# Performance work log

Measured on AMD Instinct MI355X. Metric: run time of the kernel, lower is better.

Reference implementation:

```python
import jax, jax.numpy as jnp
import numpy as np

N_NODES = 100000
N_EDGES = 1600000
D_IN = 128
D_OUT = 128


def setup_inputs() -> dict:
    key = jax.random.key(0)
    ks = jax.random.split(key, 8)
    h = jax.random.normal(ks[0], (N_NODES, D_IN), dtype=jnp.float32)
    edge_val = jax.random.uniform(ks[1], (N_EDGES,), dtype=jnp.float32)
    # Linear weights in torch layout [out, in]
    W_self = jax.random.normal(ks[2], (D_OUT, D_IN), dtype=jnp.float32) * (1.0 / np.sqrt(D_IN))
    b_self = jax.random.normal(ks[3], (D_OUT,), dtype=jnp.float32) * 0.01
    W_nb = jax.random.normal(ks[4], (D_OUT, D_IN), dtype=jnp.float32) * (1.0 / np.sqrt(D_IN))
    b_nb = jax.random.normal(ks[5], (D_OUT,), dtype=jnp.float32) * 0.01
    edge_row = jax.random.randint(ks[6], (N_EDGES,), 0, N_NODES, dtype=jnp.int64)
    edge_col = jax.random.randint(ks[7], (N_EDGES,), 0, N_NODES, dtype=jnp.int64)
    return {"h": h, "edge_val": edge_val, "W_self": W_self, "b_self": b_self,
            "W_nb": W_nb, "b_nb": b_nb, "edge_row": edge_row, "edge_col": edge_col}


def reference(h, edge_val, W_self, b_self, W_nb, b_nb, edge_row, edge_col):
    # self_h = Linear_self(h[:out_nodes]); out_nodes == N_NODES here
    self_h = h @ W_self.T + b_self  # [N, D_OUT]
    # neighbor_h = adj.spmm(h): sparse COO (row, col, val) times dense h
    msgs = edge_val[:, None] * h[edge_col]            # [E, D_IN]
    neighbor_h = jax.ops.segment_sum(msgs, edge_row, num_segments=N_NODES)  # [N, D_IN]
    out = self_h + neighbor_h @ W_nb.T + b_nb
    return out
```

## Files before the change

### kernel.cpp

```cpp
#include <hip/hip_runtime.h>


constexpr int NN = 100000;
constexpr int NE = 1600000;
constexpr int D  = 128;
constexpr int NBUCK  = 500;
constexpr int BROWS  = 200;
constexpr int BCAP   = 3584;
constexpr int CHUNK  = 2048;
constexpr int NCH    = (NE + CHUNK - 1) / CHUNK;
constexpr int GM     = 64;
constexpr int NT     = (NN + GM - 1) / GM;
constexpr int GRID   = 512;
constexpr int LP     = 132;

typedef __bf16 bf16x8 __attribute__((ext_vector_type(8)));
typedef float  f32x4  __attribute__((ext_vector_type(4)));
typedef float  f32x2  __attribute__((ext_vector_type(2)));
typedef unsigned short u16x4 __attribute__((ext_vector_type(4)));

__global__ __launch_bounds__(256) void gemm_mfma(
    const float* __restrict__ h,
    const float* __restrict__ Wself,
    const float* __restrict__ Wnb,
    const float* __restrict__ bself,
    const float* __restrict__ bnb,
    float* __restrict__ out,
    __bf16* __restrict__ tmpb)
{
    __shared__ __bf16 hs[2][GM * LP];
    const int t    = threadIdx.x;
    const int w    = t >> 6;
    const int lane = t & 63;
    const int l15  = lane & 15;
    const int quad = lane >> 4;

    bf16x8 wf[4][4];
    #pragma unroll
    for (int ns = 0; ns < 4; ++ns) {
        int wrow = w * 64 + ns * 16 + l15;
        const float* wr = (wrow < D) ? (Wself + (size_t)wrow * D)
                                     : (Wnb + (size_t)(wrow - D) * D);
        #pragma unroll
        for (int kk = 0; kk < 4; ++kk) {
            f32x4 lo = *(const f32x4*)(wr + kk * 32 + quad * 8);
            f32x4 hi = *(const f32x4*)(wr + kk * 32 + quad * 8 + 4);
            bf16x8 bb;
            #pragma unroll
            for (int j = 0; j < 4; ++j) { bb[j] = (__bf16)lo[j]; bb[4 + j] = (__bf16)hi[j]; }
            wf[ns][kk] = bb;
        }
    }
    f32x4 biasv[4];
    #pragma unroll
    for (int ns = 0; ns < 4; ++ns) {
        int col = w * 64 + ns * 16 + quad * 4;
        if (col < D) {
            f32x4 b1 = *(const f32x4*)(bself + col);
            f32x4 b2 = *(const f32x4*)(bnb + col);
            biasv[ns] = b1 + b2;
        } else biasv[ns] = (f32x4){0.f, 0.f, 0.f, 0.f};
    }

    int srow[4], scol[4];
    #pragma unroll
    for (int it = 0; it < 4; ++it) {
        int idx = it * 2048 + t * 8;
        srow[it] = idx >> 7;
        scol[it] = idx & 127;
    }

    {
        const int row0 = blockIdx.x * GM;
        #pragma unroll
        for (int it = 0; it < 4; ++it) {
            int gr = row0 + srow[it]; if (gr >= NN) gr = NN - 1;
            f32x4 lo = *(const f32x4*)(h + (size_t)gr * D + scol[it]);
            f32x4 hi = *(const f32x4*)(h + (size_t)gr * D + scol[it] + 4);
            bf16x8 v;
            #pragma unroll
            for (int j = 0; j < 4; ++j) { v[j] = (__bf16)lo[j]; v[4 + j] = (__bf16)hi[j]; }
            *(bf16x8*)(&hs[0][srow[it] * LP + scol[it]]) = v;
        }
    }
    __syncthreads();

    int buf = 0;
    for (int tile = blockIdx.x; tile < NT; tile += GRID) {
        const int row0 = tile * GM;
        const bool hasn = (tile + GRID) < NT;

        f32x4 pf[8];
        if (hasn) {
            const int nrow0 = (tile + GRID) * GM;
            #pragma unroll
            for (int it = 0; it < 4; ++it) {
                int gr = nrow0 + srow[it]; if (gr >= NN) gr = NN - 1;
                pf[it * 2]     = *(const f32x4*)(h + (size_t)gr * D + scol[it]);
                pf[it * 2 + 1] = *(const f32x4*)(h + (size_t)gr * D + scol[it] + 4);
            }
        }

        f32x4 acc[4][4];
        #pragma unroll
        for (int mi = 0; mi < 4; ++mi)
            #pragma unroll
            for (int ns = 0; ns < 4; ++ns) acc[mi][ns] = (f32x4){0.f, 0.f, 0.f, 0.f};

        const __bf16* hb = hs[buf];
        #pragma unroll
        for (int mi = 0; mi < 4; ++mi) {
            bf16x8 hf[4];
            #pragma unroll
            for (int kk = 0; kk < 4; ++kk)
                hf[kk] = *(const bf16x8*)(&hb[(mi * 16 + l15) * LP + quad * 8 + kk * 32]);
            #pragma unroll
            for (int ns = 0; ns < 4; ++ns)
                #pragma unroll
                for (int kk = 0; kk < 4; ++kk)
                    acc[mi][ns] = __builtin_amdgcn_mfma_f32_16x16x32_bf16(wf[ns][kk], hf[kk], acc[mi][ns], 0, 0, 0);
        }

        if (hasn) {
            #pragma unroll
            for (int it = 0; it < 4; ++it) {
                bf16x8 v;
                #pragma unroll
                for (int j = 0; j < 4; ++j) {
                    v[j]     = (__bf16)pf[it * 2][j];
                    v[4 + j] = (__bf16)pf[it * 2 + 1][j];
                }
                *(bf16x8*)(&hs[buf ^ 1][srow[it] * LP + scol[it]]) = v;
            }
        }
        __syncthreads();

        #pragma unroll
        for (int mi = 0; mi < 4; ++mi) {
            int row = row0 + mi * 16 + l15;
            if (row < NN) {
                if (w < 2) {
                    #pragma unroll
                    for (int ns = 0; ns < 4; ++ns) {
                        int col = w * 64 + ns * 16 + quad * 4;
                        *(f32x4*)(out + (size_t)row * D + col) = acc[mi][ns] + biasv[ns];
                    }
                } else {
                    #pragma unroll
                    for (int ns = 0; ns < 4; ++ns) {
                        int col = (w - 2) * 64 + ns * 16 + quad * 4;
                        u16x4 v;
                        #pragma unroll
                        for (int i = 0; i < 4; ++i) {
                            __bf16 b = (__bf16)acc[mi][ns][i];
                            v[i] = *(unsigned short*)&b;
                        }
                        *(u16x4*)(tmpb + (size_t)row * D + col) = v;
                    }
                }
            }
        }
        buf ^= 1;
    }
}

__global__ __launch_bounds__(256) void wc_scatter(
    const int* __restrict__ erow, const int* __restrict__ ecol,
    const float* __restrict__ eval_,
    int* __restrict__ gcount, int2* __restrict__ epair)
{
    __shared__ int  cnt[NBUCK];
    __shared__ int  lscan[NBUCK];
    __shared__ int  gbase[NBUCK];
    __shared__ int  ss[512];
    __shared__ int2 sbuf[CHUNK];
    __shared__ int  saddr[CHUNK];
    __shared__ int  s_total;

    const int t  = threadIdx.x;
    const int c0 = blockIdx.x * CHUNK;

    for (int b = t; b < NBUCK; b += 256) cnt[b] = 0;
    __syncthreads();

    int   bp[8];
    int   colr[8];
    float valr[8];
    #pragma unroll
    for (int j = 0; j < 8; ++j) {
        int e = c0 + j * 256 + t;
        if (e < NE) {
            int r   = erow[e];
            colr[j] = ecol[e];
            valr[j] = eval_[e];
            int b   = r / BROWS;
            int rlo = r - b * BROWS;
            int pos = atomicAdd(&cnt[b], 1);
            bp[j]   = b | (rlo << 9) | (pos << 17);
        } else bp[j] = -1;
    }
    __syncthreads();

    ss[t]       = (t < NBUCK)       ? cnt[t]       : 0;
    ss[t + 256] = (t + 256 < NBUCK) ? cnt[t + 256] : 0;
    __syncthreads();
    for (int off = 1; off < 512; off <<= 1) {
        int i0 = t, i1 = t + 256;
        int r0 = ss[i0] + ((i0 >= off) ? ss[i0 - off] : 0);
        int r1 = ss[i1] + ((i1 >= off) ? ss[i1 - off] : 0);
        __syncthreads();
        ss[i0] = r0; ss[i1] = r1;
        __syncthreads();
    }
    if (t < NBUCK) {
        int n = cnt[t];
        lscan[t] = ss[t] - n;
        gbase[t] = (n > 0) ? atomicAdd(&gcount[t], n) : 0;
    }
    if (t + 256 < NBUCK) {
        int n = cnt[t + 256];
        lscan[t + 256] = ss[t + 256] - n;
        gbase[t + 256] = (n > 0) ? atomicAdd(&gcount[t + 256], n) : 0;
    }
    if (t == 0) s_total = ss[511];
    __syncthreads();

    #pragma unroll
    for (int j = 0; j < 8; ++j) {
        if (bp[j] >= 0) {
            int b   = bp[j] & 511;
            int rlo = (bp[j] >> 9) & 255;
            int pos = bp[j] >> 17;
            int slot = lscan[b] + pos;
            sbuf[slot]  = make_int2(colr[j] | (rlo << 17), __float_as_int(valr[j]));
            saddr[slot] = b * BCAP + gbase[b] + pos;
        }
    }
    __syncthreads();

    int ce = s_total;
    for (int i = t; i < ce; i += 256)
        epair[saddr[i]] = sbuf[i];
}

__global__ __launch_bounds__(512) void bucket_sort(
    const int2* __restrict__ epair, const int* __restrict__ gcount,
    int2* __restrict__ epair2, int2* __restrict__ rowrange)
{
    __shared__ int  cnt[BROWS];
    __shared__ int  off2[BROWS];
    __shared__ int  cur[BROWS];
    __shared__ int  ss[256];
    __shared__ int2 sorted[BCAP];

    const int t = threadIdx.x;
    const int b = blockIdx.x;
    const int n = gcount[b];
    const int2* src = epair + (size_t)b * BCAP;

    if (t < BROWS) cnt[t] = 0;
    __syncthreads();

    int2 r[8];
    int  nr = 0;
    for (int i = t; i < n; i += 512) {
        int2 p = src[i];
        r[nr++] = p;
        atomicAdd(&cnt[(p.x >> 17) & 255], 1);
    }
    __syncthreads();

    if (t < 256) ss[t] = (t < BROWS) ? cnt[t] : 0;
    __syncthreads();
    for (int o = 1; o < 256; o <<= 1) {
        int y = 0;
        if (t < 256 && t >= o) y = ss[t - o];
        __syncthreads();
        if (t < 256) ss[t] += y;
        __syncthreads();
    }
    if (t < BROWS) {
        int v = cnt[t];
        off2[t] = ss[t] - v;
        cur[t]  = ss[t] - v;
    }
    __syncthreads();

    for (int j = 0; j < nr; ++j) {
        int slot = atomicAdd(&cur[(r[j].x >> 17) & 255], 1);
        sorted[slot] = r[j];
    }
    __syncthreads();

    const int base = b * BCAP;
    for (int i = t; i < n; i += 512)
        epair2[base + i] = sorted[i];
    if (t < BROWS) {
        int row = b * BROWS + t;
        if (row < NN)
            rowrange[row] = make_int2(base + off2[t], base + off2[t] + cnt[t]);
    }
}

__global__ __launch_bounds__(256) void aggregate(
    const __bf16* __restrict__ tmpb, const int2* __restrict__ rowrange,
    const int2* __restrict__ epair2, float* __restrict__ out,
    int row0, int nrows)
{
    int wave = row0 + ((blockIdx.x * 256 + threadIdx.x) >> 6);
    if (wave >= row0 + nrows) return;
    int lane = threadIdx.x & 63;
    int2 rr = rowrange[wave];
    int beg = __builtin_amdgcn_readfirstlane(rr.x);
    int end = __builtin_amdgcn_readfirstlane(rr.y);

    float ax[4] = {0.f, 0.f, 0.f, 0.f};
    float ay[4] = {0.f, 0.f, 0.f, 0.f};
    int e = beg;
    for (; e + 7 < end; e += 8) {
        int2 p[8];
        #pragma unroll
        for (int k = 0; k < 8; ++k) p[k] = epair2[e + k];
        #pragma unroll
        for (int k = 0; k < 8; ++k) {
            int col = p[k].x & 0x1FFFF;
            unsigned u = *(const unsigned*)(tmpb + (size_t)col * D + lane * 2);
            float v = __int_as_float(p[k].y);
            ax[k & 3] += v * __uint_as_float(u << 16);
            ay[k & 3] += v * __uint_as_float(u & 0xffff0000u);
        }
    }
    for (; e + 3 < end; e += 4) {
        int2 p[4];
        #pragma unroll
        for (int k = 0; k < 4; ++k) p[k] = epair2[e + k];
        #pragma unroll
        for (int k = 0; k < 4; ++k) {
            int col = p[k].x & 0x1FFFF;
            unsigned u = *(const unsigned*)(tmpb + (size_t)col * D + lane * 2);
            float v = __int_as_float(p[k].y);
            ax[k] += v * __uint_as_float(u << 16);
            ay[k] += v * __uint_as_float(u & 0xffff0000u);
        }
    }
    for (; e < end; ++e) {
        int2 p = epair2[e];
        int col = p.x & 0x1FFFF;
        unsigned u = *(const unsigned*)(tmpb + (size_t)col * D + lane * 2);
        float v = __int_as_float(p.y);
        ax[0] += v * __uint_as_float(u << 16);
        ay[0] += v * __uint_as_float(u & 0xffff0000u);
    }
    f32x2* o = (f32x2*)(out + (size_t)wave * D + lane * 2);
    f32x2 c = __builtin_nontemporal_load(o);
    c.x += (ax[0] + ax[1]) + (ax[2] + ax[3]);
    c.y += (ay[0] + ay[1]) + (ay[2] + ay[3]);
    __builtin_nontemporal_store(c, o);
}

extern "C" void kernel_launch(void* const* d_in, const int* in_sizes, int n_in,
                              void* d_out, int out_size, void* d_ws, size_t ws_size,
                              hipStream_t stream) {
    const float* h     = (const float*)d_in[0];
    const float* eval_ = (const float*)d_in[1];
    const float* Wself = (const float*)d_in[2];
    const float* bself = (const float*)d_in[3];
    const float* Wnb   = (const float*)d_in[4];
    const float* bnb   = (const float*)d_in[5];
    const int*   erow  = (const int*)d_in[6];
    const int*   ecol  = (const int*)d_in[7];
    float* out = (float*)d_out;

    char* p = (char*)d_ws;
    __bf16* tmpb    = (__bf16*)p;   p += (size_t)NT * GM * D * 2;
    int2*   epair   = (int2*)p;     p += (size_t)NBUCK * BCAP * 8;
    int2*   epair2  = (int2*)p;     p += (size_t)NBUCK * BCAP * 8;
    int2*   rowrange= (int2*)p;     p += (size_t)NN * 8;
    int*    gcount  = (int*)p;

    hipMemsetAsync(gcount, 0, NBUCK * 4, stream);

    gemm_mfma<<<GRID, 256, 0, stream>>>(h, Wself, Wnb, bself, bnb, out, tmpb);
    wc_scatter<<<NCH, 256, 0, stream>>>(erow, ecol, eval_, gcount, epair);
    bucket_sort<<<NBUCK, 512, 0, stream>>>(epair, gcount, epair2, rowrange);
    aggregate<<<(NN * 64) / 256, 256, 0, stream>>>(tmpb, rowrange, epair2, out, 0, NN);
}
```

Baseline: 251.8 us.

## Fuse bucket sort with neighbor aggregation, reading sorted edges from LDS

Merges the per-bucket counting sort and the SpMM aggregation into one kernel. Each block sorts its bucket's edges in shared memory, then its 8 waves each aggregate 25 rows straight from the LDS-resident sorted list. This removes the global round-trip of epair2 and rowrange and one kernel launch. In exchange, aggregation parallelism drops to 500 blocks of 8 waves each processing 25 rows sequentially, which may reduce latency hiding and cause load imbalance compared with one wave per row. The large LDS footprint also limits how many blocks can be resident per CU.

```diff
diff --git a/kernel.cpp b/kernel.cpp
--- a/kernel.cpp
+++ b/kernel.cpp
@@ -243,9 +243,9 @@
         epair[saddr[i]] = sbuf[i];
 }
 
-__global__ __launch_bounds__(512) void bucket_sort(
+__global__ __launch_bounds__(512, 4) void sort_aggregate(
     const int2* __restrict__ epair, const int* __restrict__ gcount,
-    int2* __restrict__ epair2, int2* __restrict__ rowrange)
+    const __bf16* __restrict__ tmpb, float* __restrict__ out)
 {
     __shared__ int  cnt[BROWS];
     __shared__ int  off2[BROWS];
@@ -292,70 +292,60 @@
     }
     __syncthreads();
 
-    const int base = b * BCAP;
-    for (int i = t; i < n; i += 512)
-        epair2[base + i] = sorted[i];
-    if (t < BROWS) {
-        int row = b * BROWS + t;
-        if (row < NN)
-            rowrange[row] = make_int2(base + off2[t], base + off2[t] + cnt[t]);
-    }
-}
-
-__global__ __launch_bounds__(256) void aggregate(
-    const __bf16* __restrict__ tmpb, const int2* __restrict__ rowrange,
-    const int2* __restrict__ epair2, float* __restrict__ out,
-    int row0, int nrows)
-{
-    int wave = row0 + ((blockIdx.x * 256 + threadIdx.x) >> 6);
-    if (wave >= row0 + nrows) return;
-    int lane = threadIdx.x & 63;
-    int2 rr = rowrange[wave];
-    int beg = __builtin_amdgcn_readfirstlane(rr.x);
-    int end = __builtin_amdgcn_readfirstlane(rr.y);
-
-    float ax[4] = {0.f, 0.f, 0.f, 0.f};
-    float ay[4] = {0.f, 0.f, 0.f, 0.f};
-    int e = beg;
-    for (; e + 7 < end; e += 8) {
-        int2 p[8];
-        #pragma unroll
-        for (int k = 0; k < 8; ++k) p[k] = epair2[e + k];
-        #pragma unroll
-        for (int k = 0; k < 8; ++k) {
-            int col = p[k].x & 0x1FFFF;
-            unsigned u = *(const unsigned*)(tmpb + (size_t)col * D + lane * 2);
-            float v = __int_as_float(p[k].y);
-            ax[k & 3] += v * __uint_as_float(u << 16);
-            ay[k & 3] += v * __uint_as_float(u & 0xffff0000u);
-        }
-    }
-    for (; e + 3 < end; e += 4) {
-        int2 p[4];
-        #pragma unroll
-        for (int k = 0; k < 4; ++k) p[k] = epair2[e + k];
-        #pragma unroll
-        for (int k = 0; k < 4; ++k) {
-            int col = p[k].x & 0x1FFFF;
-            unsigned u = *(const unsigned*)(tmpb + (size_t)col * D + lane * 2);
-            float v = __int_as_float(p[k].y);
-            ax[k] += v * __uint_as_float(u << 16);
-            ay[k] += v * __uint_as_float(u & 0xffff0000u);
-        }
-    }
-    for (; e < end; ++e) {
-        int2 p = epair2[e];
-        int col = p.x & 0x1FFFF;
-        unsigned u = *(const unsigned*)(tmpb + (size_t)col * D + lane * 2);
-        float v = __int_as_float(p.y);
-        ax[0] += v * __uint_as_float(u << 16);
-        ay[0] += v * __uint_as_float(u & 0xffff0000u);
-    }
-    f32x2* o = (f32x2*)(out + (size_t)wave * D + lane * 2);
-    f32x2 c = __builtin_nontemporal_load(o);
-    c.x += (ax[0] + ax[1]) + (ax[2] + ax[3]);
-    c.y += (ay[0] + ay[1]) + (ay[2] + ay[3]);
-    __builtin_nontemporal_store(c, o);
+    const int wv   = t >> 6;
+    const int lane = t & 63;
+    const __bf16* tb = tmpb + lane * 2;
+
+    for (int rl = wv * 25; rl < wv * 25 + 25; ++rl) {
+        int beg = __builtin_amdgcn_readfirstlane(off2[rl]);
+        int end = __builtin_amdgcn_readfirstlane(cur[rl]);
+        if (beg >= end) continue;
+
+        float ax[4] = {0.f, 0.f, 0.f, 0.f};
+        float ay[4] = {0.f, 0.f, 0.f, 0.f};
+        int e = beg;
+        for (; e + 7 < end; e += 8) {
+            int2 p[8];
+            #pragma unroll
+            for (int k = 0; k < 8; ++k) p[k] = sorted[e + k];
+            #pragma unroll
+            for (int k = 0; k < 8; ++k) {
+                int col = p[k].x & 0x1FFFF;
+                unsigned u = *(const unsigned*)(tb + (size_t)col * D);
+                float v = __int_as_float(p[k].y);
+                ax[k & 3] += v * __uint_as_float(u << 16);
+                ay[k & 3] += v * __uint_as_float(u & 0xffff0000u);
+            }
+        }
+        for (; e + 3 < end; e += 4) {
+            int2 p[4];
+            #pragma unroll
+            for (int k = 0; k < 4; ++k) p[k] = sorted[e + k];
+            #pragma unroll
+            for (int k = 0; k < 4; ++k) {
+                int col = p[k].x & 0x1FFFF;
+                unsigned u = *(const unsigned*)(tb + (size_t)col * D);
+                float v = __int_as_float(p[k].y);
+                ax[k] += v * __uint_as_float(u << 16);
+                ay[k] += v * __uint_as_float(u & 0xffff0000u);
+            }
+        }
+        for (; e < end; ++e) {
+            int2 p = sorted[e];
+            int col = p.x & 0x1FFFF;
+            unsigned u = *(const unsigned*)(tb + (size_t)col * D);
+            float v = __int_as_float(p.y);
+            ax[0] += v * __uint_as_float(u << 16);
+            ay[0] += v * __uint_as_float(u & 0xffff0000u);
+        }
+
+        int row = b * BROWS + rl;
+        f32x2* o = (f32x2*)(out + (size_t)row * D + lane * 2);
+        f32x2 c = __builtin_nontemporal_load(o);
+        c.x += (ax[0] + ax[1]) + (ax[2] + ax[3]);
+        c.y += (ay[0] + ay[1]) + (ay[2] + ay[3]);
+        __builtin_nontemporal_store(c, o);
+    }
 }
 
 extern "C" void kernel_launch(void* const* d_in, const int* in_sizes, int n_in,
@@ -374,14 +364,11 @@
     char* p = (char*)d_ws;
     __bf16* tmpb    = (__bf16*)p;   p += (size_t)NT * GM * D * 2;
     int2*   epair   = (int2*)p;     p += (size_t)NBUCK * BCAP * 8;
-    int2*   epair2  = (int2*)p;     p += (size_t)NBUCK * BCAP * 8;
-    int2*   rowrange= (int2*)p;     p += (size_t)NN * 8;
     int*    gcount  = (int*)p;
 
     hipMemsetAsync(gcount, 0, NBUCK * 4, stream);
 
     gemm_mfma<<<GRID, 256, 0, stream>>>(h, Wself, Wnb, bself, bnb, out, tmpb);
     wc_scatter<<<NCH, 256, 0, stream>>>(erow, ecol, eval_, gcount, epair);
-    bucket_sort<<<NBUCK, 512, 0, stream>>>(epair, gcount, epair2, rowrange);
-    aggregate<<<(NN * 64) / 256, 256, 0, stream>>>(tmpb, rowrange, epair2, out, 0, NN);
+    sort_aggregate<<<NBUCK, 512, 0, stream>>>(epair, gcount, tmpb, out);
 }
```

After: 250.8 us. No clear change (-0.4%).
